# Performance work log

Measured on AMD Instinct MI355X. Metric: run time of the kernel, lower is better.

The kernel has to match this reference:

```python
import jax, jax.numpy as jnp
import numpy as np

GROUPS = 32
EPS = 1e-5


def group_norm(x, scale, bias):
    # x: [b, v, t, s, f]; normalize per (b,v,t) sample over (channels_in_group, s)
    b, v, t, s, f = x.shape
    xg = x.reshape(b, v, t, s, GROUPS, f // GROUPS)
    mean = xg.mean(axis=(3, 5), keepdims=True)
    var = xg.var(axis=(3, 5), keepdims=True)
    xn = ((xg - mean) * jax.lax.rsqrt(var + EPS)).reshape(b, v, t, s, f)
    return xn * scale + bias


def nh_conv(x, adjc, W, b):
    # x: [b,v,t,s,f_in]; adjc: [s, k]; W: [k, f_in, f_out]; b: [f_out]
    x_nh = x[:, :, :, adjc, :]                      # [b,v,t,s,k,f_in]
    return jnp.einsum('bvtskf,kfo->bvtso', x_nh, W) + b


def setup_inputs() -> dict:
    key = jax.random.key(0)
    ks = jax.random.split(key, 12)
    B, V, T, S, F_IN, F_OUT, K = 1, 2, 2, 12288, 128, 256, 9
    x = jax.random.normal(ks[0], (B, V, T, S, F_IN), dtype=jnp.float32)
    adjc = jax.random.randint(ks[1], (S, K), 0, S, dtype=jnp.int32)
    gn1_scale = jnp.ones((F_IN,), jnp.float32)
    gn1_bias = jnp.zeros((F_IN,), jnp.float32)
    gn2_scale = jnp.ones((F_OUT,), jnp.float32)
    gn2_bias = jnp.zeros((F_OUT,), jnp.float32)
    W_skip = jax.random.normal(ks[2], (F_IN, F_OUT), jnp.float32) / np.sqrt(F_IN)
    b_skip = jnp.zeros((F_OUT,), jnp.float32)
    W1 = jax.random.normal(ks[3], (K, F_IN, F_OUT), jnp.float32) / np.sqrt(K * F_IN)
    b1 = jnp.zeros((F_OUT,), jnp.float32)
    W2 = jax.random.normal(ks[4], (K, F_OUT, F_OUT), jnp.float32) / np.sqrt(K * F_OUT)
    b2 = jnp.zeros((F_OUT,), jnp.float32)
    return dict(x=x, adjc=adjc, gn1_scale=gn1_scale, gn1_bias=gn1_bias,
                gn2_scale=gn2_scale, gn2_bias=gn2_bias, W_skip=W_skip, b_skip=b_skip,
                W1=W1, b1=b1, W2=W2, b2=b2)


def reference(x, gn1_scale, gn1_bias, gn2_scale, gn2_bias, W_skip, b_skip,
              W1, b1, W2, b2, adjc):
    # skip_layer: ProjLayer with zoom_diff=0 -> plain Linear in->out
    x_res = jnp.einsum('bvtsf,fo->bvtso', x, W_skip) + b_skip
    # norm1 + SiLU (updownconv is Identity when zooms match and in==in feats)
    h = jax.nn.silu(group_norm(x, gn1_scale, gn1_bias))
    # conv1: neighbor-gather linear [k, f_in] -> f_out
    h = nh_conv(h, adjc, W1, b1)
    # emb_layer = Identity; norm2 + SiLU
    h = jax.nn.silu(group_norm(h, gn2_scale, gn2_bias))
    # conv2 + residual
    h = nh_conv(h, adjc, W2, b2)
    return h + x_res
```

## Files before the change

### kernel.cpp

```cpp
#include <hip/hip_runtime.h>
#include <hip/hip_bf16.h>

typedef __bf16 bf16_t;
typedef __bf16 bf16x8 __attribute__((ext_vector_type(8)));
typedef float f32x4 __attribute__((ext_vector_type(4)));
typedef int i32x4 __attribute__((ext_vector_type(4)));

#define S_TOT 12288
#define F_IN 128
#define F_OUT 256
#define EPS 1e-5f

static __device__ __forceinline__ float silu_f(float v) {
  return v / (1.0f + __expf(-v));
}

static __device__ __forceinline__ void gll16(const bf16_t* g, bf16_t* l) {
  __builtin_amdgcn_global_load_lds(
      (const __attribute__((address_space(1))) void*)(const void*)g,
      (__attribute__((address_space(3))) void*)(void*)l, 16, 0, 0);
}

__global__ void prep_kernel(const float* __restrict__ W1,
                            const float* __restrict__ W2,
                            const float* __restrict__ Wsk,
                            bf16_t* __restrict__ W1p,
                            bf16_t* __restrict__ W2p,
                            bf16_t* __restrict__ Wsp,
                            const float* __restrict__ x,
                            float* __restrict__ sum1, float* __restrict__ ss1) {
  __shared__ float gs[32], gq[32];
  if (blockIdx.x < 448) {
    int w = blockIdx.x * 4 + (threadIdx.x >> 6);
    int l = threadIdx.x & 63;
    int lo = l & 15, hi = l >> 4;
    const float* src;
    bf16_t* dst;
    int fbase, obase;
    if (w < 576) {
      int kcg = w >> 4, cb = w & 15;
      int tap = kcg % 9, chunk = kcg / 9;
      src = W1 + tap * 32768;
      dst = W1p + (size_t)w * 512;
      fbase = 32 * chunk + 8 * hi; obase = 16 * cb + lo;
    } else if (w < 1728) {
      int idx = w - 576;
      int kcg = idx >> 4, cb = idx & 15;
      int tap = kcg % 9, chunk = kcg / 9;
      src = W2 + tap * 65536;
      dst = W2p + (size_t)idx * 512;
      fbase = 32 * chunk + 8 * hi; obase = 16 * cb + lo;
    } else {
      int idx = w - 1728;
      int kc = idx >> 4, cb = idx & 15;
      src = Wsk;
      dst = Wsp + (size_t)idx * 512;
      fbase = 32 * kc + 8 * hi; obase = 16 * cb + lo;
    }
    bf16x8 v;
#pragma unroll
    for (int j = 0; j < 8; ++j)
      v[j] = (bf16_t)src[(fbase + j) * 256 + obase];
    *(bf16x8*)(dst + l * 8) = v;
  } else {
    int blk = blockIdx.x - 448;
    int vt = blk & 3;
    int s0 = (blk >> 2) * 256;
    int t = threadIdx.x;
    int col = t & 31, ro = t >> 5;
    float s_ = 0.f, q_ = 0.f;
    const f32x4* xp = (const f32x4*)(x + ((size_t)vt * S_TOT + s0) * F_IN);
#pragma unroll 4
    for (int it = 0; it < 32; ++it) {
      f32x4 v = xp[(size_t)(it * 8 + ro) * 32 + col];
      s_ += v[0] + v[1] + v[2] + v[3];
      q_ += v[0]*v[0] + v[1]*v[1] + v[2]*v[2] + v[3]*v[3];
    }
    if (t < 32) { gs[t] = 0.f; gq[t] = 0.f; }
    __syncthreads();
    atomicAdd(&gs[col], s_);
    atomicAdd(&gq[col], q_);
    __syncthreads();
    if (t < 32) {
      atomicAdd(&sum1[vt * 32 + t], gs[t]);
      atomicAdd(&ss1[vt * 32 + t], gq[t]);
    }
  }
}

__global__ void apply_gn1(const float* __restrict__ x,
                          const float* __restrict__ sum1, const float* __restrict__ ss1,
                          const float* __restrict__ gs, const float* __restrict__ gb,
                          bf16_t* __restrict__ h1) {
  size_t base = ((size_t)blockIdx.x * 256 + threadIdx.x) * 8;
  int vt = (int)(base / ((size_t)S_TOT * F_IN));
  int c0 = (int)(base & (F_IN - 1));
  const f32x4* xp = (const f32x4*)(x + base);
  f32x4 v0 = xp[0], v1 = xp[1];
  float N = (float)(S_TOT * 4);
  bf16x8 o;
#pragma unroll
  for (int gi = 0; gi < 2; ++gi) {
    int g = (c0 >> 2) + gi;
    float mean = sum1[vt * 32 + g] / N;
    float var = ss1[vt * 32 + g] / N - mean * mean;
    float r = rsqrtf(var + EPS);
    f32x4 v = gi ? v1 : v0;
#pragma unroll
    for (int j = 0; j < 4; ++j) {
      int c = g * 4 + j;
      float a = r * gs[c];
      float b = gb[c] - mean * a;
      o[gi * 4 + j] = (bf16_t)silu_f(v[j] * a + b);
    }
  }
  *(bf16x8*)(h1 + base) = o;
}

__global__ void apply_gn2(bf16_t* __restrict__ h,
                          const float* __restrict__ sum_c, const float* __restrict__ ss_c,
                          const float* __restrict__ gs, const float* __restrict__ gb) {
  size_t base = ((size_t)blockIdx.x * 256 + threadIdx.x) * 8;
  int vt = (int)(base / ((size_t)S_TOT * F_OUT));
  int c0 = (int)(base & (F_OUT - 1));
  int g = c0 >> 3;
  bf16x8 v = *(const bf16x8*)(h + base);
  float sg = 0.f, qg = 0.f;
#pragma unroll
  for (int j = 0; j < 8; ++j) {
    sg += sum_c[vt * 256 + g * 8 + j];
    qg += ss_c[vt * 256 + g * 8 + j];
  }
  float N = (float)(S_TOT * 8);
  float mean = sg / N;
  float var = qg / N - mean * mean;
  float r = rsqrtf(var + EPS);
  bf16x8 o;
#pragma unroll
  for (int j = 0; j < 8; ++j) {
    int c = g * 8 + j;
    float a = r * gs[c];
    float b = gb[c] - mean * a;
    o[j] = (bf16_t)silu_f((float)v[j] * a + b);
  }
  *(bf16x8*)(h + base) = o;
}

template<int RE, int NSUB, bool XSK>
__global__ __launch_bounds__(256, 3) void conv_kernel(
    const bf16_t* __restrict__ hsrc, const bf16_t* __restrict__ Wp,
    const bf16_t* __restrict__ Wsp, const float* __restrict__ x,
    const int* __restrict__ adjc, const float* __restrict__ bias,
    const float* __restrict__ biask, bf16_t* __restrict__ outb,
    float* __restrict__ outf, float* __restrict__ sum_c, float* __restrict__ ss_c) {
  const int tid = threadIdx.x;
  const int wv = tid >> 6, l = tid & 63;
  const int lo = l & 15, hi = l >> 4;
  const int nw = wv;

  int swz = ((blockIdx.x & 7) * 96) + (blockIdx.x >> 3);
  int vt = swz / 192;
  int rem = swz - vt * 192;
  int s0 = rem * 64;

  __shared__ int adjs[576];
  __shared__ bf16_t ab[3][2048];

  for (int i = tid; i < 576; i += 256) adjs[i] = adjc[s0 * 9 + i];
  __syncthreads();

  const bf16_t* hb = hsrc + (size_t)vt * ((size_t)S_TOT * RE);
  constexpr int NMAIN = XSK ? (NSUB - 4) : NSUB;

  auto stageA = [&](int buf, int tap, int chunk) {
    int row = wv * 16 + (l >> 2);
    int segs = (l & 3) ^ ((row >> 1) & 3);
    const bf16_t* g = hb + (size_t)adjs[row * 9 + tap] * RE + chunk * 32 + segs * 8;
    gll16(g, &ab[buf][wv * 512]);
  };

  auto asmB = [&](i32x4* dst, const bf16_t* wsrc, int kcg) {
    const bf16_t* p = wsrc + (size_t)kcg * 8192 + nw * 2048 + l * 8;
    asm volatile(
        "global_load_dwordx4 %0, %4, off\n\t"
        "global_load_dwordx4 %1, %4, off offset:1024\n\t"
        "global_load_dwordx4 %2, %4, off offset:2048\n\t"
        "global_load_dwordx4 %3, %4, off offset:3072"
        : "=&v"(dst[0]), "=&v"(dst[1]), "=&v"(dst[2]), "=&v"(dst[3])
        : "v"(p));
  };

  auto stageX = [&](int buf, int sx) {
    int row = tid >> 2, q = tid & 3;
    const float* xr = x + ((size_t)vt * S_TOT + s0 + row) * F_IN + sx * 32 + q * 8;
    f32x4 xv0 = *(const f32x4*)(xr);
    f32x4 xv1 = *(const f32x4*)(xr + 4);
    bf16x8 w;
#pragma unroll
    for (int jj = 0; jj < 4; ++jj) {
      w[jj] = (bf16_t)xv0[jj];
      w[4 + jj] = (bf16_t)xv1[jj];
    }
    *(bf16x8*)(&ab[buf][row * 32 + ((q ^ ((row >> 1) & 3)) << 3)]) = w;
  };

  f32x4 acc[4][4] = {};
  auto compute = [&](int buf, const i32x4* bv) {
    bf16x8 afr[4];
#pragma unroll
    for (int mi = 0; mi < 4; ++mi) {
      int rr = mi * 16 + lo;
      afr[mi] = *(const bf16x8*)(&ab[buf][rr * 32 + ((hi ^ ((rr >> 1) & 3)) << 3)]);
    }
    __builtin_amdgcn_s_setprio(1);
#pragma unroll
    for (int mi = 0; mi < 4; ++mi)
#pragma unroll
      for (int ni = 0; ni < 4; ++ni)
        acc[mi][ni] = __builtin_amdgcn_mfma_f32_16x16x32_bf16(
            afr[mi], __builtin_bit_cast(bf16x8, bv[ni]), acc[mi][ni], 0, 0, 0);
    __builtin_amdgcn_s_setprio(0);
  };

  i32x4 b0[4], b1[4];
  stageA(0, 0, 0);
  asmB(b0, Wp, 0);
  stageA(1, 1, 0);
  int bcur3 = 0, bstg3 = 2;
  int t2 = 2, c2 = 0;

  for (int s = 0; s < NMAIN - 2; s += 2) {
    asmB(b1, Wp, s + 1);
    asm volatile("s_waitcnt vmcnt(5)" ::: "memory");
    __builtin_amdgcn_s_barrier();
    __builtin_amdgcn_sched_barrier(0);
    stageA(bstg3, t2, c2);
    if (++t2 == 9) { t2 = 0; ++c2; }
    compute(bcur3, b0);
    bcur3 = (bcur3 == 2) ? 0 : bcur3 + 1;
    bstg3 = (bstg3 == 2) ? 0 : bstg3 + 1;
    asmB(b0, Wp, s + 2);
    asm volatile("s_waitcnt vmcnt(5)" ::: "memory");
    __builtin_amdgcn_s_barrier();
    __builtin_amdgcn_sched_barrier(0);
    stageA(bstg3, t2, c2);
    if (++t2 == 9) { t2 = 0; ++c2; }
    compute(bcur3, b1);
    bcur3 = (bcur3 == 2) ? 0 : bcur3 + 1;
    bstg3 = (bstg3 == 2) ? 0 : bstg3 + 1;
  }
  asmB(b1, Wp, NMAIN - 1);
  asm volatile("s_waitcnt vmcnt(5)" ::: "memory");
  __builtin_amdgcn_s_barrier();
  __builtin_amdgcn_sched_barrier(0);
  compute(bcur3, b0);
  bcur3 = (bcur3 == 2) ? 0 : bcur3 + 1;
  asm volatile("s_waitcnt vmcnt(0)" ::: "memory");
  __builtin_amdgcn_s_barrier();
  __builtin_amdgcn_sched_barrier(0);
  compute(bcur3, b1);

  if (XSK) {
#pragma unroll
    for (int sx = 0; sx < 4; ++sx) {
      int tb = sx & 1;
      __syncthreads();
      stageX(tb, sx);
      if (sx & 1) asmB(b1, Wsp, sx); else asmB(b0, Wsp, sx);
      asm volatile("s_waitcnt vmcnt(0)" ::: "memory");
      __syncthreads();
      __builtin_amdgcn_sched_barrier(0);
      compute(tb, (sx & 1) ? (const i32x4*)b1 : (const i32x4*)b0);
    }
  }

  if (!XSK) {
    bf16_t* ob = outb + ((size_t)vt * S_TOT + s0) * 256;
#pragma unroll
    for (int ni = 0; ni < 4; ++ni) {
      int o = nw * 64 + ni * 16 + lo;
      float bv = bias[o];
      float s_ = 0.f, q_ = 0.f;
#pragma unroll
      for (int mi = 0; mi < 4; ++mi)
#pragma unroll
        for (int r2 = 0; r2 < 4; ++r2) {
          int srow = mi * 16 + hi * 4 + r2;
          float v = acc[mi][ni][r2] + bv;
          ob[(size_t)srow * 256 + o] = (bf16_t)v;
          s_ += v; q_ += v * v;
        }
      s_ += __shfl_xor(s_, 16); s_ += __shfl_xor(s_, 32);
      q_ += __shfl_xor(q_, 16); q_ += __shfl_xor(q_, 32);
      if (hi == 0) {
        atomicAdd(&sum_c[vt * 256 + o], s_);
        atomicAdd(&ss_c[vt * 256 + o], q_);
      }
    }
  } else {
    float* of = outf + ((size_t)vt * S_TOT + s0) * 256;
#pragma unroll
    for (int ni = 0; ni < 4; ++ni) {
      int o = nw * 64 + ni * 16 + lo;
      float bv = bias[o] + biask[o];
#pragma unroll
      for (int mi = 0; mi < 4; ++mi)
#pragma unroll
        for (int r2 = 0; r2 < 4; ++r2) {
          int srow = mi * 16 + hi * 4 + r2;
          of[(size_t)srow * 256 + o] = acc[mi][ni][r2] + bv;
        }
    }
  }
}

extern "C" void kernel_launch(void* const* d_in, const int* in_sizes, int n_in,
                              void* d_out, int out_size, void* d_ws, size_t ws_size,
                              hipStream_t stream) {
  const float* x      = (const float*)d_in[0];
  const int*   adjc   = (const int*)d_in[1];
  const float* gn1_s  = (const float*)d_in[2];
  const float* gn1_b  = (const float*)d_in[3];
  const float* gn2_s  = (const float*)d_in[4];
  const float* gn2_b  = (const float*)d_in[5];
  const float* W_skip = (const float*)d_in[6];
  const float* b_skip = (const float*)d_in[7];
  const float* W1     = (const float*)d_in[8];
  const float* b1     = (const float*)d_in[9];
  const float* W2     = (const float*)d_in[10];
  const float* b2     = (const float*)d_in[11];
  float* out = (float*)d_out;

  float* sum1  = (float*)d_ws;
  float* ss1   = sum1 + 128;
  float* sum_c = ss1 + 128;
  float* ss_c  = sum_c + 1024;
  float* pad   = ss_c + 1024;
  bf16_t* W1p  = (bf16_t*)(pad + 3072);
  bf16_t* W2p  = W1p + 294912;
  bf16_t* Wsp  = W2p + 589824;
  bf16_t* h1   = Wsp + 32768;
  bf16_t* out1 = h1 + 6291456;

  hipMemsetAsync(sum1, 0, (128 + 128 + 1024 + 1024) * sizeof(float), stream);
  prep_kernel<<<640, 256, 0, stream>>>(W1, W2, W_skip, W1p, W2p, Wsp, x, sum1, ss1);
  apply_gn1<<<3072, 256, 0, stream>>>(x, sum1, ss1, gn1_s, gn1_b, h1);
  conv_kernel<128, 36, false><<<768, 256, 0, stream>>>(
      h1, W1p, nullptr, nullptr, adjc, b1, nullptr, out1, nullptr, sum_c, ss_c);
  apply_gn2<<<6144, 256, 0, stream>>>(out1, sum_c, ss_c, gn2_s, gn2_b);
  conv_kernel<256, 76, true><<<768, 256, 0, stream>>>(
      out1, W2p, Wsp, x, adjc, b2, b_skip, nullptr, out, nullptr, nullptr);
}
```

Baseline: 140.6 us.

## Enlarge conv tile to 192 rows per block, one block per CU

Triples the row tile of each conv block from 64 to 192 output rows, so each weight fragment loaded into registers feeds 12 MFMA row tiles instead of 4. This cuts global weight traffic per output by a factor of three. The grid shrinks from 768 to 256 blocks (one per CU on a 256-CU part) and launch bounds drop to one block per SM. Each thread now holds 48 accumulators, which lowers occupancy and leaves less room to hide latency from the gathered A loads.

Result: slower. 179.8 us (+27.9%).

```diff
diff --git a/kernel.cpp b/kernel.cpp
--- a/kernel.cpp
+++ b/kernel.cpp
@@ -147,7 +147,7 @@
 }
 
 template<int RE, int NSUB, bool XSK>
-__global__ __launch_bounds__(256, 3) void conv_kernel(
+__global__ __launch_bounds__(256, 1) void conv_kernel(
     const bf16_t* __restrict__ hsrc, const bf16_t* __restrict__ Wp,
     const bf16_t* __restrict__ Wsp, const float* __restrict__ x,
     const int* __restrict__ adjc, const float* __restrict__ bias,
@@ -158,25 +158,29 @@
   const int lo = l & 15, hi = l >> 4;
   const int nw = wv;
 
-  int swz = ((blockIdx.x & 7) * 96) + (blockIdx.x >> 3);
-  int vt = swz / 192;
-  int rem = swz - vt * 192;
-  int s0 = rem * 64;
-
-  __shared__ int adjs[576];
-  __shared__ bf16_t ab[3][2048];
-
-  for (int i = tid; i < 576; i += 256) adjs[i] = adjc[s0 * 9 + i];
+  int swz = ((blockIdx.x & 7) << 5) + (blockIdx.x >> 3);
+  int vt = swz >> 6;
+  int rem = swz & 63;
+  int s0 = rem * 192;
+
+  __shared__ int adjs[1728];
+  __shared__ bf16_t ab[3][6144];
+
+  for (int i = tid; i < 1728; i += 256) adjs[i] = adjc[s0 * 9 + i];
   __syncthreads();
 
   const bf16_t* hb = hsrc + (size_t)vt * ((size_t)S_TOT * RE);
   constexpr int NMAIN = XSK ? (NSUB - 4) : NSUB;
 
-  auto stageA = [&](int buf, int tap, int chunk) {
-    int row = wv * 16 + (l >> 2);
-    int segs = (l & 3) ^ ((row >> 1) & 3);
-    const bf16_t* g = hb + (size_t)adjs[row * 9 + tap] * RE + chunk * 32 + segs * 8;
-    gll16(g, &ab[buf][wv * 512]);
+  auto stageA = [&](int buf, int s) {
+    int tap = s % 9, chunk = s / 9;
+#pragma unroll
+    for (int j2 = 0; j2 < 3; ++j2) {
+      int row = wv * 48 + j2 * 16 + (l >> 2);
+      int segs = (l & 3) ^ ((row >> 1) & 3);
+      const bf16_t* g = hb + (size_t)adjs[row * 9 + tap] * RE + chunk * 32 + segs * 8;
+      gll16(g, &ab[buf][(wv * 48 + j2 * 16) * 32]);
+    }
   };
 
   auto asmB = [&](i32x4* dst, const bf16_t* wsrc, int kcg) {
@@ -191,66 +195,64 @@
   };
 
   auto stageX = [&](int buf, int sx) {
-    int row = tid >> 2, q = tid & 3;
-    const float* xr = x + ((size_t)vt * S_TOT + s0 + row) * F_IN + sx * 32 + q * 8;
-    f32x4 xv0 = *(const f32x4*)(xr);
-    f32x4 xv1 = *(const f32x4*)(xr + 4);
-    bf16x8 w;
-#pragma unroll
-    for (int jj = 0; jj < 4; ++jj) {
-      w[jj] = (bf16_t)xv0[jj];
-      w[4 + jj] = (bf16_t)xv1[jj];
-    }
-    *(bf16x8*)(&ab[buf][row * 32 + ((q ^ ((row >> 1) & 3)) << 3)]) = w;
+#pragma unroll
+    for (int i = 0; i < 3; ++i) {
+      int row = i * 64 + (tid >> 2);
+      int q = tid & 3;
+      const float* xr = x + ((size_t)vt * S_TOT + s0 + row) * F_IN + sx * 32 + q * 8;
+      f32x4 xv0 = *(const f32x4*)(xr);
+      f32x4 xv1 = *(const f32x4*)(xr + 4);
+      bf16x8 w;
+#pragma unroll
+      for (int jj = 0; jj < 4; ++jj) {
+        w[jj] = (bf16_t)xv0[jj];
+        w[4 + jj] = (bf16_t)xv1[jj];
+      }
+      *(bf16x8*)(&ab[buf][row * 32 + ((q ^ ((row >> 1) & 3)) << 3)]) = w;
+    }
   };
 
-  f32x4 acc[4][4] = {};
+  f32x4 acc[12][4] = {};
   auto compute = [&](int buf, const i32x4* bv) {
-    bf16x8 afr[4];
-#pragma unroll
-    for (int mi = 0; mi < 4; ++mi) {
+    __builtin_amdgcn_s_setprio(1);
+#pragma unroll
+    for (int mi = 0; mi < 12; ++mi) {
       int rr = mi * 16 + lo;
-      afr[mi] = *(const bf16x8*)(&ab[buf][rr * 32 + ((hi ^ ((rr >> 1) & 3)) << 3)]);
-    }
-    __builtin_amdgcn_s_setprio(1);
-#pragma unroll
-    for (int mi = 0; mi < 4; ++mi)
+      bf16x8 afr = *(const bf16x8*)(&ab[buf][rr * 32 + ((hi ^ ((rr >> 1) & 3)) << 3)]);
 #pragma unroll
       for (int ni = 0; ni < 4; ++ni)
         acc[mi][ni] = __builtin_amdgcn_mfma_f32_16x16x32_bf16(
-            afr[mi], __builtin_bit_cast(bf16x8, bv[ni]), acc[mi][ni], 0, 0, 0);
+            afr, __builtin_bit_cast(bf16x8, bv[ni]), acc[mi][ni], 0, 0, 0);
+    }
     __builtin_amdgcn_s_setprio(0);
   };
 
   i32x4 b0[4], b1[4];
-  stageA(0, 0, 0);
+  stageA(0, 0);
   asmB(b0, Wp, 0);
-  stageA(1, 1, 0);
+  stageA(1, 1);
   int bcur3 = 0, bstg3 = 2;
-  int t2 = 2, c2 = 0;
 
   for (int s = 0; s < NMAIN - 2; s += 2) {
     asmB(b1, Wp, s + 1);
-    asm volatile("s_waitcnt vmcnt(5)" ::: "memory");
+    asm volatile("s_waitcnt vmcnt(7)" ::: "memory");
     __builtin_amdgcn_s_barrier();
     __builtin_amdgcn_sched_barrier(0);
-    stageA(bstg3, t2, c2);
-    if (++t2 == 9) { t2 = 0; ++c2; }
+    stageA(bstg3, s + 2);
     compute(bcur3, b0);
     bcur3 = (bcur3 == 2) ? 0 : bcur3 + 1;
     bstg3 = (bstg3 == 2) ? 0 : bstg3 + 1;
     asmB(b0, Wp, s + 2);
-    asm volatile("s_waitcnt vmcnt(5)" ::: "memory");
+    asm volatile("s_waitcnt vmcnt(7)" ::: "memory");
     __builtin_amdgcn_s_barrier();
     __builtin_amdgcn_sched_barrier(0);
-    stageA(bstg3, t2, c2);
-    if (++t2 == 9) { t2 = 0; ++c2; }
+    stageA(bstg3, s + 3);
     compute(bcur3, b1);
     bcur3 = (bcur3 == 2) ? 0 : bcur3 + 1;
     bstg3 = (bstg3 == 2) ? 0 : bstg3 + 1;
   }
   asmB(b1, Wp, NMAIN - 1);
-  asm volatile("s_waitcnt vmcnt(5)" ::: "memory");
+  asm volatile("s_waitcnt vmcnt(7)" ::: "memory");
   __builtin_amdgcn_s_barrier();
   __builtin_amdgcn_sched_barrier(0);
   compute(bcur3, b0);
@@ -282,7 +284,7 @@
       float bv = bias[o];
       float s_ = 0.f, q_ = 0.f;
 #pragma unroll
-      for (int mi = 0; mi < 4; ++mi)
+      for (int mi = 0; mi < 12; ++mi)
 #pragma unroll
         for (int r2 = 0; r2 < 4; ++r2) {
           int srow = mi * 16 + hi * 4 + r2;
@@ -304,7 +306,7 @@
       int o = nw * 64 + ni * 16 + lo;
       float bv = bias[o] + biask[o];
 #pragma unroll
-      for (int mi = 0; mi < 4; ++mi)
+      for (int mi = 0; mi < 12; ++mi)
 #pragma unroll
         for (int r2 = 0; r2 < 4; ++r2) {
           int srow = mi * 16 + hi * 4 + r2;
@@ -345,9 +347,9 @@
   hipMemsetAsync(sum1, 0, (128 + 128 + 1024 + 1024) * sizeof(float), stream);
   prep_kernel<<<640, 256, 0, stream>>>(W1, W2, W_skip, W1p, W2p, Wsp, x, sum1, ss1);
   apply_gn1<<<3072, 256, 0, stream>>>(x, sum1, ss1, gn1_s, gn1_b, h1);
-  conv_kernel<128, 36, false><<<768, 256, 0, stream>>>(
+  conv_kernel<128, 36, false><<<256, 256, 0, stream>>>(
       h1, W1p, nullptr, nullptr, adjc, b1, nullptr, out1, nullptr, sum_c, ss_c);
   apply_gn2<<<6144, 256, 0, stream>>>(out1, sum_c, ss_c, gn2_s, gn2_b);
-  conv_kernel<256, 76, true><<<768, 256, 0, stream>>>(
+  conv_kernel<256, 76, true><<<256, 256, 0, stream>>>(
       out1, W2p, Wsp, x, adjc, b2, b_skip, nullptr, out, nullptr, nullptr);
 }
```
